# Performance work log

Hardware: AMD Instinct MI355X
Metric: run time of the kernel (lower is better)

The kernel has to match this reference:

```python
import jax, jax.numpy as jnp
import numpy as np

B, N, D = 8, 1024, 512
H, F = 8, 2048
Dh = D // H
EPS = 1e-5
NEG = -1.0e9


def _layernorm(x, g, b):
    mu = jnp.mean(x, axis=-1, keepdims=True)
    var = jnp.mean(jnp.square(x - mu), axis=-1, keepdims=True)
    return (x - mu) * jax.lax.rsqrt(var + EPS) * g + b


def setup_inputs() -> dict:
    key = jax.random.key(0)
    ks = jax.random.split(key, 8)
    s = 0.02  # weight init scale
    return {
        "x": jax.random.normal(ks[0], (B, N, D), jnp.float32),
        "adjacency_logits": jax.random.normal(ks[1], (N, N), jnp.float32),
        "candidate_edge_mask": jax.random.randint(ks[2], (N, N), 0, 2).astype(jnp.bool_),
        "Wq": jax.random.normal(ks[3], (D, D), jnp.float32) * s,
        "Wk": jax.random.normal(ks[4], (D, D), jnp.float32) * s,
        "Wv": jax.random.normal(ks[5], (D, D), jnp.float32) * s,
        "Wo": jax.random.normal(ks[6], (D, D), jnp.float32) * s,
        "W1": jax.random.normal(jax.random.fold_in(key, 10), (F, D), jnp.float32) * s,
        "b1": jnp.zeros((F,), jnp.float32),
        "W2": jax.random.normal(jax.random.fold_in(key, 11), (D, F), jnp.float32) * s,
        "b2": jnp.zeros((D,), jnp.float32),
        "g_ln1": jnp.ones((D,), jnp.float32),
        "beta_ln1": jnp.zeros((D,), jnp.float32),
        "g_ln2": jnp.ones((D,), jnp.float32),
        "beta_ln2": jnp.zeros((D,), jnp.float32),
    }


def reference(x, adjacency_logits, candidate_edge_mask, Wq, Wk, Wv, Wo,
              W1, b1, W2, b2, g_ln1, beta_ln1, g_ln2, beta_ln2):
    b, n, d = x.shape
    # projections: torch Linear is x @ W^T  -> [B,H,N,Dh]
    def proj(W):
        return jnp.einsum('bnd,ed->bne', x, W).reshape(b, n, H, Dh).transpose(0, 2, 1, 3)
    q, k, v = proj(Wq), proj(Wk), proj(Wv)
    scale = 1.0 / jnp.sqrt(jnp.float32(Dh))
    scores = jnp.einsum('bhqd,bhkd->bhqk', q, k) * scale
    scores = scores + adjacency_logits[None, None]
    mask = candidate_edge_mask[None, None]  # [1,1,N,N]
    scores = jnp.where(mask, scores, NEG)
    attn = jax.nn.softmax(scores, axis=-1)
    attn = jnp.where(mask, attn, 0.0)
    ctx = jnp.einsum('bhqk,bhkd->bhqd', attn, v)
    ctx = ctx.transpose(0, 2, 1, 3).reshape(b, n, d)
    attn_out = jnp.einsum('bnd,ed->bne', ctx, Wo)
    z = _layernorm(x + attn_out, g_ln1, beta_ln1)
    h = jax.nn.relu(jnp.einsum('bnd,fd->bnf', z, W1) + b1)
    z_ffn = jnp.einsum('bnf,df->bnd', h, W2) + b2
    out = _layernorm(z + z_ffn, g_ln2, beta_ln2)
    return out, attn.mean(axis=1)
```

## Files before the change

kernel.cpp:

```cpp
#include <hip/hip_runtime.h>
#include <math.h>
#include <stdint.h>


using bf16_t = __bf16;
typedef __attribute__((__ext_vector_type__(8))) __bf16 bf16x8;
typedef __attribute__((__ext_vector_type__(4))) __bf16 bf16x4;
typedef __attribute__((__ext_vector_type__(4))) float  f32x4;

#define DEVI __device__ __forceinline__

DEVI f32x4 mfma16(bf16x8 a, bf16x8 b, f32x4 c) {
  return __builtin_amdgcn_mfma_f32_16x16x32_bf16(a, b, c, 0, 0, 0);
}

DEVI void gload_lds16(const void* g, void* l) {
  __builtin_amdgcn_global_load_lds(
      (const __attribute__((address_space(1))) uint32_t*)g,
      (__attribute__((address_space(3))) uint32_t*)l, 16, 0, 0);
}

#define EPSC  (1e-5f)
#define QSCALE 0.18033688f

__global__ __launch_bounds__(256) void k_cvtall(const float* __restrict__ x,
                                                const float* __restrict__ wq,
                                                const float* __restrict__ wk,
                                                const float* __restrict__ wv,
                                                const float* __restrict__ wo,
                                                const float* __restrict__ w1,
                                                const float* __restrict__ w2,
                                                const float* __restrict__ adj,
                                                const int* __restrict__ msk,
                                                bf16_t* __restrict__ ox,
                                                bf16_t* __restrict__ owq,
                                                bf16_t* __restrict__ owk,
                                                bf16_t* __restrict__ owv,
                                                bf16_t* __restrict__ owo,
                                                bf16_t* __restrict__ ow1,
                                                bf16_t* __restrict__ ow2,
                                                bf16_t* __restrict__ eadjP) {
  int blk = blockIdx.x;
  if (blk >= 7168) {
    int row  = (blk - 7168) * 4 + (threadIdx.x >> 6);
    int lane = threadIdx.x & 63;
    for (int i = 0; i < 16; i++) {
      int c = lane + 64 * i;
      size_t idx = (size_t)row * 1024 + c;
      float a = adj[idx];
      bool valid = (msk[idx] != 0);
      int pos = (c & ~63) + ((c & 15) << 2) + ((c >> 4) & 3);
      eadjP[(size_t)row * 1024 + pos] = valid ? (__bf16)__expf(a) : (__bf16)0.f;
    }
    return;
  }
  const float* src; bf16_t* dst; int base;
  if (blk < 4096)      { src = x;  dst = ox;  base = blk; }
  else {
    blk -= 4096;
    if      (blk < 256)  { src = wq; dst = owq; base = blk; }
    else if (blk < 512)  { src = wk; dst = owk; base = blk - 256; }
    else if (blk < 768)  { src = wv; dst = owv; base = blk - 512; }
    else if (blk < 1024) { src = wo; dst = owo; base = blk - 768; }
    else if (blk < 2048) { src = w1; dst = ow1; base = blk - 1024; }
    else                 { src = w2; dst = ow2; base = blk - 2048; }
  }
  int i = base * 256 + threadIdx.x;
  float4 v = ((const float4*)src)[i];
  bf16x4 o = { (__bf16)v.x, (__bf16)v.y, (__bf16)v.z, (__bf16)v.w };
  ((bf16x4*)dst)[i] = o;
}

template<int EPI, int NSPLIT>
__global__ __launch_bounds__(256) void k_gemm(const bf16_t* __restrict__ A,
                                              const bf16_t* __restrict__ B,
                                              int K, int nbx,
                                              const float* __restrict__ bias,
                                              bf16_t* __restrict__ outb,
                                              float* __restrict__ outf,
                                              int out_ncols) {
  __shared__ bf16_t lA[2][4096];
  __shared__ bf16_t lB[2][4096];
  int bid = blockIdx.x;
  int bps = 64 * nbx;
  int split = bid / bps, r = bid - split * bps;
  int nb = r % nbx, mb = r / nbx;
  int KS = K / NSPLIT;
  const bf16_t* Ab = A + (size_t)split * KS;
  const bf16_t* Bb = B + (size_t)split * KS;
  int tid = threadIdx.x, wid = tid >> 6, lane = tid & 63;
  int l16 = lane & 15, g = lane >> 4;
  int wr = wid >> 1, wc = wid & 1;
  int rowbase = mb * 128, c0 = nb * 128;

  int dA0 = wid * 2048 + lane * 16;
  int rA0 = dA0 >> 6;
  int cbA = ((dA0 >> 4) & 3) ^ (rA0 & 3);
  const bf16_t* Asrc0 = Ab + (size_t)(rowbase + rA0) * K + cbA * 8;
  const bf16_t* Asrc1 = Ab + (size_t)(rowbase + rA0 + 16) * K + cbA * 8;
  const bf16_t* Bsrc0 = Bb + (size_t)(c0 + rA0) * K + cbA * 8;
  const bf16_t* Bsrc1 = Bb + (size_t)(c0 + rA0 + 16) * K + cbA * 8;

  f32x4 acc[4][4];
#pragma unroll
  for (int m = 0; m < 4; m++)
#pragma unroll
    for (int n = 0; n < 4; n++) acc[m][n] = (f32x4){0.f, 0.f, 0.f, 0.f};

  gload_lds16(Asrc0, (char*)&lA[0][0] + wid * 2048);
  gload_lds16(Asrc1, (char*)&lA[0][0] + wid * 2048 + 1024);
  gload_lds16(Bsrc0, (char*)&lB[0][0] + wid * 2048);
  gload_lds16(Bsrc1, (char*)&lB[0][0] + wid * 2048 + 1024);
  __syncthreads();

  for (int k0 = 0; k0 < KS; k0 += 32) {
    int buf = (k0 >> 5) & 1;
    if (k0 + 32 < KS) {
      gload_lds16(Asrc0 + k0 + 32, (char*)&lA[buf ^ 1][0] + wid * 2048);
      gload_lds16(Asrc1 + k0 + 32, (char*)&lA[buf ^ 1][0] + wid * 2048 + 1024);
      gload_lds16(Bsrc0 + k0 + 32, (char*)&lB[buf ^ 1][0] + wid * 2048);
      gload_lds16(Bsrc1 + k0 + 32, (char*)&lB[buf ^ 1][0] + wid * 2048 + 1024);
    }
    const char* cA = (const char*)&lA[buf][0];
    const char* cB = (const char*)&lB[buf][0];
    bf16x8 af[4], bq[4];
#pragma unroll
    for (int m = 0; m < 4; m++) {
      int row = wr * 64 + m * 16 + l16;
      af[m] = *(const bf16x8*)(cA + row * 64 + ((g ^ (row & 3)) << 4));
    }
#pragma unroll
    for (int n = 0; n < 4; n++) {
      int row = wc * 64 + n * 16 + l16;
      bq[n] = *(const bf16x8*)(cB + row * 64 + ((g ^ (row & 3)) << 4));
    }
#pragma unroll
    for (int m = 0; m < 4; m++)
#pragma unroll
      for (int n = 0; n < 4; n++) acc[m][n] = mfma16(af[m], bq[n], acc[m][n]);
    __syncthreads();
  }

  int which = c0 / out_ncols;
  int cloc0 = c0 - which * out_ncols;
  size_t obase = (size_t)which * 8192 * out_ncols +
                 (size_t)split * 8192 * out_ncols * (NSPLIT > 1 ? 1 : 0);
  float osc = (EPI == 0 && which == 0) ? QSCALE : 1.0f;
#pragma unroll
  for (int n = 0; n < 4; n++) {
    int col = cloc0 + wc * 64 + n * 16 + l16;
    float bv = (EPI >= 1 && bias && split == 0) ? bias[col] : 0.f;
#pragma unroll
    for (int m = 0; m < 4; m++)
#pragma unroll
      for (int j = 0; j < 4; j++) {
        int row = rowbase + wr * 64 + m * 16 + g * 4 + j;
        float v = acc[m][n][j] + bv;
        size_t idx = obase + (size_t)row * out_ncols + col;
        if (EPI == 1) outb[idx] = (__bf16)fmaxf(v, 0.f);
        else if (EPI == 0) outb[idx] = (__bf16)(v * osc);
        else outf[idx] = v;
      }
  }
}

__global__ __launch_bounds__(256) void k_resln(const float* __restrict__ gin,
                                               int nsplit,
                                               const float* __restrict__ residf,
                                               const bf16_t* __restrict__ residb,
                                               const float* __restrict__ gam,
                                               const float* __restrict__ bet,
                                               float* __restrict__ outf,
                                               bf16_t* __restrict__ outb) {
  const size_t GS = (size_t)8192 * 512;
  int row = blockIdx.x * 4 + (threadIdx.x >> 6);
  int lane = threadIdx.x & 63;
  const float* gp = gin + (size_t)row * 512;
  float4 a0 = ((const float4*)gp)[lane];
  float4 a1 = ((const float4*)gp)[lane + 64];
  for (int s = 1; s < nsplit; s++) {
    const float* gp2 = gp + s * GS;
    float4 r0 = ((const float4*)gp2)[lane];
    float4 r1 = ((const float4*)gp2)[lane + 64];
    a0.x += r0.x; a0.y += r0.y; a0.z += r0.z; a0.w += r0.w;
    a1.x += r1.x; a1.y += r1.y; a1.z += r1.z; a1.w += r1.w;
  }
  if (residf) {
    const float* rp = residf + (size_t)row * 512;
    float4 r0 = ((const float4*)rp)[lane];
    float4 r1 = ((const float4*)rp)[lane + 64];
    a0.x += r0.x; a0.y += r0.y; a0.z += r0.z; a0.w += r0.w;
    a1.x += r1.x; a1.y += r1.y; a1.z += r1.z; a1.w += r1.w;
  } else {
    const bf16_t* rp = residb + (size_t)row * 512;
    bf16x4 r0 = ((const bf16x4*)rp)[lane];
    bf16x4 r1 = ((const bf16x4*)rp)[lane + 64];
    a0.x += (float)r0[0]; a0.y += (float)r0[1]; a0.z += (float)r0[2]; a0.w += (float)r0[3];
    a1.x += (float)r1[0]; a1.y += (float)r1[1]; a1.z += (float)r1[2]; a1.w += (float)r1[3];
  }
  float s = a0.x + a0.y + a0.z + a0.w + a1.x + a1.y + a1.z + a1.w;
  for (int off = 1; off < 64; off <<= 1) s += __shfl_xor(s, off);
  float mu = s * (1.f / 512.f);
  float sq = (a0.x - mu) * (a0.x - mu) + (a0.y - mu) * (a0.y - mu) +
             (a0.z - mu) * (a0.z - mu) + (a0.w - mu) * (a0.w - mu) +
             (a1.x - mu) * (a1.x - mu) + (a1.y - mu) * (a1.y - mu) +
             (a1.z - mu) * (a1.z - mu) + (a1.w - mu) * (a1.w - mu);
  for (int off = 1; off < 64; off <<= 1) sq += __shfl_xor(sq, off);
  float rs = rsqrtf(sq * (1.f / 512.f) + EPSC);

  float4 g0 = ((const float4*)gam)[lane], g1v = ((const float4*)gam)[lane + 64];
  float4 b0 = ((const float4*)bet)[lane], b1v = ((const float4*)bet)[lane + 64];
  float4 o0, o1;
  o0.x = (a0.x - mu) * rs * g0.x + b0.x;  o0.y = (a0.y - mu) * rs * g0.y + b0.y;
  o0.z = (a0.z - mu) * rs * g0.z + b0.z;  o0.w = (a0.w - mu) * rs * g0.w + b0.w;
  o1.x = (a1.x - mu) * rs * g1v.x + b1v.x; o1.y = (a1.y - mu) * rs * g1v.y + b1v.y;
  o1.z = (a1.z - mu) * rs * g1v.z + b1v.z; o1.w = (a1.w - mu) * rs * g1v.w + b1v.w;
  if (outf) {
    float* op = outf + (size_t)row * 512;
    ((float4*)op)[lane] = o0;
    ((float4*)op)[lane + 64] = o1;
  }
  if (outb) {
    bf16_t* op = outb + (size_t)row * 512;
    bf16x4 q0 = { (__bf16)o0.x, (__bf16)o0.y, (__bf16)o0.z, (__bf16)o0.w };
    bf16x4 q1 = { (__bf16)o1.x, (__bf16)o1.y, (__bf16)o1.z, (__bf16)o1.w };
    ((bf16x4*)op)[lane] = q0;
    ((bf16x4*)op)[lane + 64] = q1;
  }
}

__global__ __launch_bounds__(256) void k_vtrans_knorm(const bf16_t* __restrict__ v,
                                                      bf16_t* __restrict__ vT,
                                                      const bf16_t* __restrict__ kk,
                                                      float* __restrict__ kmax) {
  __shared__ bf16_t t[64 * 66];
  __shared__ float red[4];
  int bid = blockIdx.x;
  int tid = threadIdx.x, wid = tid >> 6, lane = tid & 63;
  if (bid < 1024) {
    int nt = bid & 15, h = (bid >> 4) & 7, b = bid >> 7;
    for (int i = 0; i < 16; i++) {
      int n = wid * 16 + i;
      t[lane * 66 + n] = v[(size_t)(b * 1024 + nt * 64 + n) * 512 + h * 64 + lane];
    }
    __syncthreads();
    for (int i = 0; i < 16; i++) {
      int d = wid * 16 + i;
      vT[(size_t)((b * 8 + h) * 64 + d) * 1024 + nt * 64 + lane] = t[d * 66 + lane];
    }
  } else {
    int bh = bid - 1024;
    int b = bh >> 3, h = bh & 7;
    float mx = 0.f;
    for (int n = tid; n < 1024; n += 256) {
      const bf16_t* kp = kk + (size_t)(b * 1024 + n) * 512 + h * 64;
      float ss = 0.f;
#pragma unroll
      for (int vv = 0; vv < 8; vv++) {
        bf16x8 kv = *(const bf16x8*)(kp + vv * 8);
#pragma unroll
        for (int e = 0; e < 8; e++) { float f = (float)kv[e]; ss += f * f; }
      }
      mx = fmaxf(mx, ss);
    }
    for (int off = 1; off < 64; off <<= 1) mx = fmaxf(mx, __shfl_xor(mx, off));
    if (lane == 0) red[wid] = mx;
    __syncthreads();
    if (tid == 0) kmax[bh] = sqrtf(fmaxf(fmaxf(red[0], red[1]), fmaxf(red[2], red[3])));
  }
}

__global__ __launch_bounds__(512) void k_attn_ctx(const bf16_t* __restrict__ q,
                                                  const bf16_t* __restrict__ kk,
                                                  const bf16_t* __restrict__ vT,
                                                  const bf16_t* __restrict__ eadjP,
                                                  const float* __restrict__ kmax,
                                                  bf16_t* __restrict__ ctx,
                                                  float* __restrict__ crl) {
  __shared__ bf16_t ldsK[2][4096];
  __shared__ bf16_t ldsV[2][4096];
  __shared__ bf16_t pt[8][16 * 68];
  int bid = blockIdx.x;
  int qt = bid >> 6, h = bid & 7, b = (bid >> 3) & 7;
  int tid = threadIdx.x, wid = tid >> 6, lane = tid & 63;
  int l16 = lane & 15, g = lane >> 4;
  int qg0 = qt * 128 + wid * 16;
  int kvbase = (b * 8 + h) * 64;

  int d0 = wid * 1024 + lane * 16;
  int row0 = d0 >> 7;
  int cb0 = ((d0 >> 4) & 7) ^ (row0 & 7);
  const bf16_t* ksrc = kk + (size_t)(b * 1024) * 512 + h * 64;
  const bf16_t* vsrc = vT + (size_t)kvbase * 1024;

  auto stage = [&](int buf, int kc0) {
    gload_lds16(ksrc + (size_t)(kc0 + row0) * 512 + cb0 * 8, &ldsK[buf][wid * 512]);
    gload_lds16(vsrc + (size_t)row0 * 1024 + kc0 + cb0 * 8, &ldsV[buf][wid * 512]);
  };

  const bf16_t* qp = q + (size_t)(b * 1024 + qg0 + l16) * 512 + h * 64 + 8 * g;
  bf16x8 aq0 = *(const bf16x8*)qp;
  bf16x8 aq1 = *(const bf16x8*)(qp + 32);

  float kmaxv = kmax[b * 8 + h];
  float ssq = 0.f;
#pragma unroll
  for (int e = 0; e < 8; e++) {
    float f0 = (float)aq0[e], f1 = (float)aq1[e];
    ssq += f0 * f0 + f1 * f1;
  }
  ssq += __shfl_xor(ssq, 16);
  ssq += __shfl_xor(ssq, 32);
  float Cn = sqrtf(ssq) * kmaxv;
  f32x4 negC;
#pragma unroll
  for (int j = 0; j < 4; j++) negC[j] = -__shfl(Cn, g * 4 + j);

  f32x4 cacc[4];
#pragma unroll
  for (int d = 0; d < 4; d++) cacc[d] = (f32x4){0.f, 0.f, 0.f, 0.f};
  float ls[4] = {0.f, 0.f, 0.f, 0.f};
  bf16_t* myp = pt[wid];
  int rph = l16 & 7;
  const bf16_t* erowP = eadjP + (size_t)(qg0 + g * 4) * 1024 + l16 * 4;

  bf16x4 ea0[4], ea1[4];
  auto loadEA = [&](bf16x4 (&d)[4], int kc0) {
#pragma unroll
    for (int j = 0; j < 4; j++)
      d[j] = *(const bf16x4*)(erowP + (size_t)j * 1024 + kc0);
  };

  auto cbar = [&]() {
    __builtin_amdgcn_sched_barrier(0);
    asm volatile("s_waitcnt vmcnt(4) lgkmcnt(0)" ::: "memory");
    __builtin_amdgcn_sched_barrier(0);
    __builtin_amdgcn_s_barrier();
    __builtin_amdgcn_sched_barrier(0);
  };

  auto tile = [&](int kt, int buf, bf16x4 (&eaC)[4], bf16x4 (&eaN)[4]) {
    int kc0 = kt * 64;
    int ktn = (kt + 1 < 16) ? kt + 1 : 15;
    stage(buf ^ 1, ktn * 64);
    loadEA(eaN, ktn * 64);

    const char* curK = (const char*)ldsK[buf];
    const char* curV = (const char*)ldsV[buf];

#pragma unroll
    for (int cg = 0; cg < 4; cg++) {
      const char* krow = curK + ((cg * 16 + l16) << 7);
      bf16x8 k0 = *(const bf16x8*)(krow + ((g ^ rph) << 4));
      bf16x8 k1 = *(const bf16x8*)(krow + (((g + 4) ^ rph) << 4));
      __builtin_amdgcn_s_setprio(1);
      f32x4 s = mfma16(aq0, k0, negC);
      s = mfma16(aq1, k1, s);
      __builtin_amdgcn_s_setprio(0);
#pragma unroll
      for (int j = 0; j < 4; j++) {
        float p = (float)eaC[j][cg] * exp2f(s[j]);
        ls[j] += p;
        myp[(g * 4 + j) * 68 + cg * 16 + l16] = (__bf16)p;
      }
    }
#pragma unroll
    for (int half = 0; half < 2; half++) {
      bf16x8 pa = *(const bf16x8*)(myp + l16 * 68 + half * 32 + 8 * g);
      __builtin_amdgcn_s_setprio(1);
#pragma unroll
      for (int dg = 0; dg < 4; dg++) {
        const char* vrow = curV + ((dg * 16 + l16) << 7);
        bf16x8 vv = *(const bf16x8*)(vrow + (((g + half * 4) ^ rph) << 4));
        cacc[dg] = mfma16(pa, vv, cacc[dg]);
      }
      __builtin_amdgcn_s_setprio(0);
    }
    cbar();
  };

  stage(0, 0);
  loadEA(ea0, 0);
  cbar();

  for (int k2 = 0; k2 < 8; k2++) {
    tile(2 * k2,     0, ea0, ea1);
    tile(2 * k2 + 1, 1, ea1, ea0);
  }

#pragma unroll
  for (int j = 0; j < 4; j++)
    for (int off = 1; off < 16; off <<= 1) ls[j] += __shfl_xor(ls[j], off);
  float rc[4];
#pragma unroll
  for (int j = 0; j < 4; j++) rc[j] = (ls[j] > 0.f) ? (1.f / ls[j]) : 0.f;

#pragma unroll
  for (int dg = 0; dg < 4; dg++)
#pragma unroll
    for (int j = 0; j < 4; j++) {
      int row = qg0 + g * 4 + j;
      ctx[(size_t)(b * 1024 + row) * 512 + h * 64 + dg * 16 + l16] =
          (__bf16)(cacc[dg][j] * rc[j]);
    }
  if (l16 == 0) {
#pragma unroll
    for (int j = 0; j < 4; j++) {
      int li = (b * 8 + h) * 1024 + qg0 + g * 4 + j;
      crl[li] = (ls[j] > 0.f) ? (-negC[j] + __log2f(ls[j])) : 1.0e30f;
    }
  }
}

__global__ __launch_bounds__(256, 4) void k_attn_mean(const bf16_t* __restrict__ q,
                                                      const bf16_t* __restrict__ kk,
                                                      const bf16_t* __restrict__ eadjP,
                                                      const float* __restrict__ crl,
                                                      float* __restrict__ mout) {
  __shared__ bf16_t lds[4][2][2048];
  int bid = blockIdx.x;
  int kq = bid & 7, qt = (bid >> 3) & 15, b = bid >> 7;
  int tid = threadIdx.x, wid = tid >> 6, lane = tid & 63;
  int l16 = lane & 15, g = lane >> 4;
  int qg0 = qt * 64 + wid * 16;
  int kbase = kq * 128;
  int rl = lane >> 3;
  int cb = (lane & 7) ^ rl;
  const bf16_t* ksrc = kk + (size_t)(b * 1024 + kbase) * 512;

  auto stage = [&](int t) {
    int h = t >> 2, c = t & 3;
    char* dst = (char*)&lds[wid][t & 1][0];
    const bf16_t* sp = ksrc + (size_t)(c * 32 + rl) * 512 + h * 64 + cb * 8;
#pragma unroll
    for (int i = 0; i < 4; i++)
      gload_lds16(sp + (size_t)i * 8 * 512, dst + i * 1024);
  };

  f32x4 macc[8];
#pragma unroll
  for (int kg = 0; kg < 8; kg++) macc[kg] = (f32x4){0.f, 0.f, 0.f, 0.f};

  stage(0);

  for (int h = 0; h < 8; h++) {
    const bf16_t* qp = q + (size_t)(b * 1024 + qg0 + l16) * 512 + h * 64 + 8 * g;
    bf16x8 aq0 = *(const bf16x8*)qp;
    bf16x8 aq1 = *(const bf16x8*)(qp + 32);
    f32x4 CR = *(const f32x4*)(crl + (b * 8 + h) * 1024 + qg0 + g * 4);
    f32x4 negCR = (f32x4){-CR[0], -CR[1], -CR[2], -CR[3]};
#pragma unroll
    for (int c = 0; c < 4; c++) {
      int t = h * 4 + c;
      __builtin_amdgcn_sched_barrier(0);
      if (t < 31) {
        stage(t + 1);
        __builtin_amdgcn_sched_barrier(0);
        asm volatile("s_waitcnt vmcnt(4)" ::: "memory");
      } else {
        asm volatile("s_waitcnt vmcnt(0)" ::: "memory");
      }
      __builtin_amdgcn_sched_barrier(0);
      const char* cK = (const char*)&lds[wid][t & 1][0];
#pragma unroll
      for (int cg = 0; cg < 2; cg++) {
        const char* krow = cK + ((cg * 16 + l16) << 7);
        bf16x8 k0 = *(const bf16x8*)(krow + ((g ^ (l16 & 7)) << 4));
        bf16x8 k1 = *(const bf16x8*)(krow + (((g + 4) ^ (l16 & 7)) << 4));
        __builtin_amdgcn_s_setprio(1);
        f32x4 s = mfma16(aq0, k0, negCR);
        s = mfma16(aq1, k1, s);
        __builtin_amdgcn_s_setprio(0);
        int kg = c * 2 + cg;
#pragma unroll
        for (int j = 0; j < 4; j++)
          macc[kg][j] += exp2f(s[j]);
      }
    }
  }

#pragma unroll
  for (int kg = 0; kg < 8; kg++)
#pragma unroll
    for (int j = 0; j < 4; j++) {
      size_t row = qg0 + g * 4 + j;
      size_t off = row * 1024 + kbase + kg * 16 + l16;
      size_t poff = row * 1024 + 64 * (kq * 2 + (kg >> 2)) + l16 * 4 + (kg & 3);
      mout[(size_t)b * 1048576 + off] = macc[kg][j] * (float)eadjP[poff] * 0.125f;
    }
}

extern "C" void kernel_launch(void* const* d_in, const int* in_sizes, int n_in,
                              void* d_out, int out_size, void* d_ws, size_t ws_size,
                              hipStream_t stream) {
  (void)in_sizes; (void)n_in; (void)out_size; (void)ws_size;
  const float* x   = (const float*)d_in[0];
  const float* adj = (const float*)d_in[1];
  const int*   msk = (const int*)d_in[2];
  const float* Wq  = (const float*)d_in[3];
  const float* Wk  = (const float*)d_in[4];
  const float* Wv  = (const float*)d_in[5];
  const float* Wo  = (const float*)d_in[6];
  const float* W1  = (const float*)d_in[7];
  const float* b1  = (const float*)d_in[8];
  const float* W2  = (const float*)d_in[9];
  const float* b2  = (const float*)d_in[10];
  const float* g1  = (const float*)d_in[11];
  const float* be1 = (const float*)d_in[12];
  const float* g2  = (const float*)d_in[13];
  const float* be2 = (const float*)d_in[14];

  float* out  = (float*)d_out;
  float* mout = out + (size_t)8 * 1024 * 512;

  char* ws = (char*)d_ws;
  const size_t MB = 1024 * 1024;
  bf16_t* wqb = (bf16_t*)(ws);
  bf16_t* wkb = (bf16_t*)(ws + 512 * 1024);
  bf16_t* wvb = (bf16_t*)(ws + 1 * MB);
  bf16_t* wob = (bf16_t*)(ws + 3 * MB / 2);
  bf16_t* w1b = (bf16_t*)(ws + 2 * MB);
  bf16_t* w2b = (bf16_t*)(ws + 4 * MB);
  float*  crl  = (float*)(ws + 6 * MB + 256 * 1024);
  float*  kmax = (float*)(ws + 6 * MB + 768 * 1024);
  bf16_t* xb   = (bf16_t*)(ws + 8 * MB);
  bf16_t* ctx  = xb;
  bf16_t* zb   = xb;
  bf16_t* qb   = (bf16_t*)(ws + 16 * MB);
  bf16_t* kb   = (bf16_t*)(ws + 24 * MB);
  bf16_t* vb   = (bf16_t*)(ws + 32 * MB);
  bf16_t* vT   = (bf16_t*)(ws + 40 * MB);
  float*  gout1 = (float*)(ws + 16 * MB);
  bf16_t* hb    = (bf16_t*)(ws + 16 * MB);
  float*  gout2 = (float*)(ws + 44 * MB);
  bf16_t* eadjP = (bf16_t*)(ws + 72 * MB);

  k_cvtall<<<7424, 256, 0, stream>>>(x, Wq, Wk, Wv, Wo, W1, W2, adj, msk,
                                     xb, wqb, wkb, wvb, wob, w1b, w2b, eadjP);

  k_gemm<0, 1><<<64 * 12, 256, 0, stream>>>(xb, wqb, 512, 12, nullptr, qb, nullptr, 512);
  k_vtrans_knorm<<<1088, 256, 0, stream>>>(vb, vT, kb, kmax);

  k_attn_ctx<<<512, 512, 0, stream>>>(qb, kb, vT, eadjP, kmax, ctx, crl);
  k_attn_mean<<<1024, 256, 0, stream>>>(qb, kb, eadjP, crl, mout);

  k_gemm<2, 2><<<2 * 64 * 4, 256, 0, stream>>>(ctx, wob, 512, 4, nullptr, nullptr, gout1, 512);
  k_resln<<<2048, 256, 0, stream>>>(gout1, 2, x, nullptr, g1, be1, nullptr, zb);
  k_gemm<1, 1><<<64 * 16, 256, 0, stream>>>(zb, w1b, 512, 16, b1, hb, nullptr, 2048);
  k_gemm<2, 2><<<2 * 64 * 4, 256, 0, stream>>>(hb, w2b, 2048, 4, b2, nullptr, gout2, 512);
  k_resln<<<2048, 256, 0, stream>>>(gout2, 2, nullptr, zb, g2, be2, out, nullptr);
}
```

Baseline: 228.6 us.

## Compute transposed QK^T scores so P stays in registers, skipping LDS round-trip

Swaps the MFMA operand order so each lane holds scores for a single query row across keys. The exp(adj) table and V^T are permuted to match that layout, so probabilities can be packed straight into bf16x8 A-operands for the PV MFMA without the per-wave LDS staging buffer. Row-sum reduction and the max-shift constant collapse to one scalar per lane. The attn-mean kernel also gets vectorized float4 output stores and wider eadj loads. The cost is a more intricate permuted layout that all producers and consumers must agree on, and any mismatch would corrupt results.

```diff
diff --git a/kernel.cpp b/kernel.cpp
--- a/kernel.cpp
+++ b/kernel.cpp
@@ -39,7 +39,7 @@
                                                 bf16_t* __restrict__ owo,
                                                 bf16_t* __restrict__ ow1,
                                                 bf16_t* __restrict__ ow2,
-                                                bf16_t* __restrict__ eadjP) {
+                                                bf16_t* __restrict__ eadjT) {
   int blk = blockIdx.x;
   if (blk >= 7168) {
     int row  = (blk - 7168) * 4 + (threadIdx.x >> 6);
@@ -49,8 +49,8 @@
       size_t idx = (size_t)row * 1024 + c;
       float a = adj[idx];
       bool valid = (msk[idx] != 0);
-      int pos = (c & ~63) + ((c & 15) << 2) + ((c >> 4) & 3);
-      eadjP[(size_t)row * 1024 + pos] = valid ? (__bf16)__expf(a) : (__bf16)0.f;
+      int pos = (c & ~63) + (((c >> 2) & 3) << 4) + (((c >> 4) & 3) << 2) + (c & 3);
+      eadjT[(size_t)row * 1024 + pos] = valid ? (__bf16)__expf(a) : (__bf16)0.f;
     }
     return;
   }
@@ -244,9 +244,10 @@
       t[lane * 66 + n] = v[(size_t)(b * 1024 + nt * 64 + n) * 512 + h * 64 + lane];
     }
     __syncthreads();
+    int pi = (lane & 32) + (((lane >> 2) & 3) << 3) + (((lane >> 4) & 1) << 2) + (lane & 3);
     for (int i = 0; i < 16; i++) {
       int d = wid * 16 + i;
-      vT[(size_t)((b * 8 + h) * 64 + d) * 1024 + nt * 64 + lane] = t[d * 66 + lane];
+      vT[(size_t)((b * 8 + h) * 64 + d) * 1024 + nt * 64 + pi] = t[d * 66 + lane];
     }
   } else {
     int bh = bid - 1024;
@@ -273,13 +274,12 @@
 __global__ __launch_bounds__(512) void k_attn_ctx(const bf16_t* __restrict__ q,
                                                   const bf16_t* __restrict__ kk,
                                                   const bf16_t* __restrict__ vT,
-                                                  const bf16_t* __restrict__ eadjP,
+                                                  const bf16_t* __restrict__ eadjT,
                                                   const float* __restrict__ kmax,
                                                   bf16_t* __restrict__ ctx,
                                                   float* __restrict__ crl) {
   __shared__ bf16_t ldsK[2][4096];
   __shared__ bf16_t ldsV[2][4096];
-  __shared__ bf16_t pt[8][16 * 68];
   int bid = blockIdx.x;
   int qt = bid >> 6, h = bid & 7, b = (bid >> 3) & 7;
   int tid = threadIdx.x, wid = tid >> 6, lane = tid & 63;
@@ -312,35 +312,30 @@
   ssq += __shfl_xor(ssq, 16);
   ssq += __shfl_xor(ssq, 32);
   float Cn = sqrtf(ssq) * kmaxv;
-  f32x4 negC;
-#pragma unroll
-  for (int j = 0; j < 4; j++) negC[j] = -__shfl(Cn, g * 4 + j);
+  f32x4 negC4 = (f32x4){-Cn, -Cn, -Cn, -Cn};
 
   f32x4 cacc[4];
 #pragma unroll
   for (int d = 0; d < 4; d++) cacc[d] = (f32x4){0.f, 0.f, 0.f, 0.f};
-  float ls[4] = {0.f, 0.f, 0.f, 0.f};
-  bf16_t* myp = pt[wid];
+  float ls = 0.f;
   int rph = l16 & 7;
-  const bf16_t* erowP = eadjP + (size_t)(qg0 + g * 4) * 1024 + l16 * 4;
-
-  bf16x4 ea0[4], ea1[4];
-  auto loadEA = [&](bf16x4 (&d)[4], int kc0) {
-#pragma unroll
-    for (int j = 0; j < 4; j++)
-      d[j] = *(const bf16x4*)(erowP + (size_t)j * 1024 + kc0);
+  const bf16_t* erowT = eadjT + (size_t)(qg0 + l16) * 1024 + g * 16;
+
+  bf16x8 eaA[2], eaB[2];
+  auto loadEA = [&](bf16x8 (&d)[2], int kc0) {
+    d[0] = *(const bf16x8*)(erowT + kc0);
+    d[1] = *(const bf16x8*)(erowT + kc0 + 8);
   };
 
   auto cbar = [&]() {
     __builtin_amdgcn_sched_barrier(0);
-    asm volatile("s_waitcnt vmcnt(4) lgkmcnt(0)" ::: "memory");
+    asm volatile("s_waitcnt vmcnt(2) lgkmcnt(0)" ::: "memory");
     __builtin_amdgcn_sched_barrier(0);
     __builtin_amdgcn_s_barrier();
     __builtin_amdgcn_sched_barrier(0);
   };
 
-  auto tile = [&](int kt, int buf, bf16x4 (&eaC)[4], bf16x4 (&eaN)[4]) {
-    int kc0 = kt * 64;
+  auto tile = [&](int kt, int buf, bf16x8 (&eaC)[2], bf16x8 (&eaN)[2]) {
     int ktn = (kt + 1 < 16) ? kt + 1 : 15;
     stage(buf ^ 1, ktn * 64);
     loadEA(eaN, ktn * 64);
@@ -348,25 +343,27 @@
     const char* curK = (const char*)ldsK[buf];
     const char* curV = (const char*)ldsV[buf];
 
+    bf16x8 pa0, pa1;
 #pragma unroll
     for (int cg = 0; cg < 4; cg++) {
       const char* krow = curK + ((cg * 16 + l16) << 7);
       bf16x8 k0 = *(const bf16x8*)(krow + ((g ^ rph) << 4));
       bf16x8 k1 = *(const bf16x8*)(krow + (((g + 4) ^ rph) << 4));
       __builtin_amdgcn_s_setprio(1);
-      f32x4 s = mfma16(aq0, k0, negC);
-      s = mfma16(aq1, k1, s);
+      f32x4 s = mfma16(k0, aq0, negC4);
+      s = mfma16(k1, aq1, s);
       __builtin_amdgcn_s_setprio(0);
 #pragma unroll
       for (int j = 0; j < 4; j++) {
-        float p = (float)eaC[j][cg] * exp2f(s[j]);
-        ls[j] += p;
-        myp[(g * 4 + j) * 68 + cg * 16 + l16] = (__bf16)p;
+        float p = (float)eaC[cg >> 1][(cg & 1) * 4 + j] * exp2f(s[j]);
+        ls += p;
+        if (cg < 2) pa0[cg * 4 + j] = (__bf16)p;
+        else        pa1[(cg - 2) * 4 + j] = (__bf16)p;
       }
     }
 #pragma unroll
     for (int half = 0; half < 2; half++) {
-      bf16x8 pa = *(const bf16x8*)(myp + l16 * 68 + half * 32 + 8 * g);
+      bf16x8 pa = half ? pa1 : pa0;
       __builtin_amdgcn_s_setprio(1);
 #pragma unroll
       for (int dg = 0; dg < 4; dg++) {
@@ -380,20 +377,20 @@
   };
 
   stage(0, 0);
-  loadEA(ea0, 0);
+  loadEA(eaA, 0);
   cbar();
 
   for (int k2 = 0; k2 < 8; k2++) {
-    tile(2 * k2,     0, ea0, ea1);
-    tile(2 * k2 + 1, 1, ea1, ea0);
-  }
-
-#pragma unroll
-  for (int j = 0; j < 4; j++)
-    for (int off = 1; off < 16; off <<= 1) ls[j] += __shfl_xor(ls[j], off);
-  float rc[4];
-#pragma unroll
-  for (int j = 0; j < 4; j++) rc[j] = (ls[j] > 0.f) ? (1.f / ls[j]) : 0.f;
+    tile(2 * k2,     0, eaA, eaB);
+    tile(2 * k2 + 1, 1, eaB, eaA);
+  }
+
+  ls += __shfl_xor(ls, 16);
+  ls += __shfl_xor(ls, 32);
+  float rcv = (ls > 0.f) ? (1.f / ls) : 0.f;
+  float rcj[4];
+#pragma unroll
+  for (int j = 0; j < 4; j++) rcj[j] = __shfl(rcv, g * 4 + j);
 
 #pragma unroll
   for (int dg = 0; dg < 4; dg++)
@@ -401,20 +398,17 @@
     for (int j = 0; j < 4; j++) {
       int row = qg0 + g * 4 + j;
       ctx[(size_t)(b * 1024 + row) * 512 + h * 64 + dg * 16 + l16] =
-          (__bf16)(cacc[dg][j] * rc[j]);
-    }
-  if (l16 == 0) {
-#pragma unroll
-    for (int j = 0; j < 4; j++) {
-      int li = (b * 8 + h) * 1024 + qg0 + g * 4 + j;
-      crl[li] = (ls[j] > 0.f) ? (-negC[j] + __log2f(ls[j])) : 1.0e30f;
-    }
+          (__bf16)(cacc[dg][j] * rcj[j]);
+    }
+  if (lane < 16) {
+    int li = (b * 8 + h) * 1024 + qg0 + lane;
+    crl[li] = (ls > 0.f) ? (Cn + __log2f(ls)) : 1.0e30f;
   }
 }
 
 __global__ __launch_bounds__(256, 4) void k_attn_mean(const bf16_t* __restrict__ q,
                                                       const bf16_t* __restrict__ kk,
-                                                      const bf16_t* __restrict__ eadjP,
+                                                      const bf16_t* __restrict__ eadjT,
                                                       const float* __restrict__ crl,
                                                       float* __restrict__ mout) {
   __shared__ bf16_t lds[4][2][2048];
@@ -447,8 +441,8 @@
     const bf16_t* qp = q + (size_t)(b * 1024 + qg0 + l16) * 512 + h * 64 + 8 * g;
     bf16x8 aq0 = *(const bf16x8*)qp;
     bf16x8 aq1 = *(const bf16x8*)(qp + 32);
-    f32x4 CR = *(const f32x4*)(crl + (b * 8 + h) * 1024 + qg0 + g * 4);
-    f32x4 negCR = (f32x4){-CR[0], -CR[1], -CR[2], -CR[3]};
+    float CRs = crl[(b * 8 + h) * 1024 + qg0 + l16];
+    f32x4 negCR4 = (f32x4){-CRs, -CRs, -CRs, -CRs};
 #pragma unroll
     for (int c = 0; c < 4; c++) {
       int t = h * 4 + c;
@@ -468,8 +462,8 @@
         bf16x8 k0 = *(const bf16x8*)(krow + ((g ^ (l16 & 7)) << 4));
         bf16x8 k1 = *(const bf16x8*)(krow + (((g + 4) ^ (l16 & 7)) << 4));
         __builtin_amdgcn_s_setprio(1);
-        f32x4 s = mfma16(aq0, k0, negCR);
-        s = mfma16(aq1, k1, s);
+        f32x4 s = mfma16(k0, aq0, negCR4);
+        s = mfma16(k1, aq1, s);
         __builtin_amdgcn_s_setprio(0);
         int kg = c * 2 + cg;
 #pragma unroll
@@ -479,15 +473,21 @@
     }
   }
 
-#pragma unroll
-  for (int kg = 0; kg < 8; kg++)
-#pragma unroll
-    for (int j = 0; j < 4; j++) {
-      size_t row = qg0 + g * 4 + j;
-      size_t off = row * 1024 + kbase + kg * 16 + l16;
-      size_t poff = row * 1024 + 64 * (kq * 2 + (kg >> 2)) + l16 * 4 + (kg & 3);
-      mout[(size_t)b * 1048576 + off] = macc[kg][j] * (float)eadjP[poff] * 0.125f;
-    }
+  const bf16_t* erowT = eadjT + (size_t)(qg0 + l16) * 1024 + kbase + g * 16;
+  bf16x8 eA0 = *(const bf16x8*)(erowT);
+  bf16x8 eA1 = *(const bf16x8*)(erowT + 8);
+  bf16x8 eB0 = *(const bf16x8*)(erowT + 64);
+  bf16x8 eB1 = *(const bf16x8*)(erowT + 72);
+  float* mrow = mout + (size_t)b * 1048576 + (size_t)(qg0 + l16) * 1024 + kbase;
+#pragma unroll
+  for (int kg = 0; kg < 8; kg++) {
+    bf16x8 eg = (kg < 2) ? eA0 : (kg < 4) ? eA1 : (kg < 6) ? eB0 : eB1;
+    f32x4 mv;
+#pragma unroll
+    for (int j = 0; j < 4; j++)
+      mv[j] = macc[kg][j] * (float)eg[(kg & 1) * 4 + j] * 0.125f;
+    *(f32x4*)(mrow + kg * 16 + g * 4) = mv;
+  }
 }
 
 extern "C" void kernel_launch(void* const* d_in, const int* in_sizes, int n_in,
@@ -533,16 +533,16 @@
   float*  gout1 = (float*)(ws + 16 * MB);
   bf16_t* hb    = (bf16_t*)(ws + 16 * MB);
   float*  gout2 = (float*)(ws + 44 * MB);
-  bf16_t* eadjP = (bf16_t*)(ws + 72 * MB);
+  bf16_t* eadjT = (bf16_t*)(ws + 72 * MB);
 
   k_cvtall<<<7424, 256, 0, stream>>>(x, Wq, Wk, Wv, Wo, W1, W2, adj, msk,
-                                     xb, wqb, wkb, wvb, wob, w1b, w2b, eadjP);
+                                     xb, wqb, wkb, wvb, wob, w1b, w2b, eadjT);
 
   k_gemm<0, 1><<<64 * 12, 256, 0, stream>>>(xb, wqb, 512, 12, nullptr, qb, nullptr, 512);
   k_vtrans_knorm<<<1088, 256, 0, stream>>>(vb, vT, kb, kmax);
 
-  k_attn_ctx<<<512, 512, 0, stream>>>(qb, kb, vT, eadjP, kmax, ctx, crl);
-  k_attn_mean<<<1024, 256, 0, stream>>>(qb, kb, eadjP, crl, mout);
+  k_attn_ctx<<<512, 512, 0, stream>>>(qb, kb, vT, eadjT, kmax, ctx, crl);
+  k_attn_mean<<<1024, 256, 0, stream>>>(qb, kb, eadjT, crl, mout);
 
   k_gemm<2, 2><<<2 * 64 * 4, 256, 0, stream>>>(ctx, wob, 512, 4, nullptr, nullptr, gout1, 512);
   k_resln<<<2048, 256, 0, stream>>>(gout1, 2, x, nullptr, g1, be1, nullptr, zb);
```

Measured after the change: 218.2 us. 1.05x faster.
